# Kernel optimization log

Hardware: AMD Instinct MI355X
Metric: run time of the kernel (lower is better)

The kernel has to match this reference:

```python
import jax, jax.numpy as jnp
import numpy as np
from math import comb

ORDER = 16
K = ORDER + 1  # 17
D = 32         # input_dim
P = 20         # num_perm
N = 24576


def _bernstein(X, order):
    # X: [N, D] in [0,1] -> Bernstein basis [N, D, order+1]
    ks = jnp.arange(order + 1)
    binoms = jnp.array([comb(order, k) for k in range(order + 1)], jnp.float32)
    Xe = X[..., None]
    return (Xe ** ks) * ((1.0 - Xe) ** (order - ks)) * binoms


def _prior_sc_np(order):
    # prior_adjusting: sqrt(inv(B(x)^2) @ 1) at x = linspace(0,1,order+1)
    ks = np.arange(order + 1)
    binoms = np.array([comb(order, k) for k in range(order + 1)], np.float64)
    x = np.linspace(0.0, 1.0, order + 1)[:, None]
    B = (x ** ks) * ((1.0 - x) ** (order - ks)) * binoms  # (K, K)
    Pmat = np.linalg.inv(B ** 2)
    v = Pmat @ np.ones((order + 1, 1))
    return np.sqrt(np.maximum(v, 1e-12)).astype(np.float32)  # (K, 1)


def setup_inputs() -> dict:
    key = jax.random.key(0)
    k1, k2, k3, k4, k5 = jax.random.split(key, 5)
    mean_mu = (0.0001 / P) ** (1.0 / D)
    Xnew = jax.random.uniform(k1, (N, D), dtype=jnp.float32)
    meanw0 = mean_mu + 0.1 * jax.random.normal(k2, (P, 1, K), dtype=jnp.float32)
    meanw = mean_mu + 0.1 * jax.random.normal(k3, (D - 1, P, K, K), dtype=jnp.float32)
    varw0 = -0.1 + 0.1 * jax.random.normal(k4, (P, 1, K), dtype=jnp.float32)
    varw = -0.1 + 0.1 * jax.random.normal(k5, (D - 1, P, K, K), dtype=jnp.float32)
    rng = np.random.default_rng(0)
    perm = jnp.array(np.stack([rng.permutation(D) for _ in range(P)]), jnp.int32)
    prior_sc = jnp.array(_prior_sc_np(ORDER))
    post_prec = jnp.full((P,), float(P), dtype=jnp.float32)
    return {"Xnew": Xnew, "meanw0": meanw0, "meanw": meanw, "varw0": varw0,
            "varw": varw, "prior_sc": prior_sc, "post_prec": post_prec, "perm": perm}


def reference(Xnew, meanw0, meanw, varw0, varw, prior_sc, post_prec, perm):
    Bout = _bernstein(Xnew, ORDER)                      # (N, D, K)
    outB = jnp.transpose(Bout[:, perm], (1, 0, 2, 3))   # (P, N, D, K)
    outBd = jnp.transpose(outB, (2, 0, 1, 3))           # (D, P, N, K)

    # f_mean: ones(P,N,1) @ meanw0 -> broadcast of meanw0 rows; then chained small matmuls
    f0 = meanw0[:, 0, :][:, None, :] * outBd[0]         # (P, N, K)

    def mean_step(f, inputs):
        W, b = inputs                                   # W: (P,K,K), b: (P,N,K)
        return jnp.einsum('pnk,pkj->pnj', f, W) * b, None

    f, _ = jax.lax.scan(mean_step, f0, (meanw, outBd[1:]))
    f_mean = jnp.sum(jnp.sum(f, axis=-1), axis=0)[:, None]  # (N, 1)

    # f_var: weights exp(varw)*prior_sc^2.T, basis squared
    sc2 = (prior_sc ** 2)[:, 0]                          # (K,)
    g0 = (jnp.exp(varw0) * sc2)[:, 0, :][:, None, :] * outBd[0] ** 2  # (P, N, K)

    def var_step(g, inputs):
        Vw, b = inputs
        return jnp.einsum('pnk,pkj->pnj', g, jnp.exp(Vw) * sc2) * (b ** 2), None

    g, _ = jax.lax.scan(var_step, g0, (varw, outBd[1:]))
    f_var = jnp.sum(jnp.sum(g, axis=-1) / post_prec[:, None], axis=0)[:, None]  # (N, 1)
    return f_mean, f_var
```

## Files before the change

kernel.cpp:

```cpp
#include <hip/hip_runtime.h>

#define NN 24576
#define DD 32
#define KK 17
#define PP 20

__device__ __forceinline__ void bern17(float x, float* b) {
    const float binom[KK] = {1.f, 16.f, 120.f, 560.f, 1820.f, 4368.f, 8008.f, 11440.f,
                             12870.f, 11440.f, 8008.f, 4368.f, 1820.f, 560.f, 120.f, 16.f, 1.f};
    const float y = 1.0f - x;
    b[0] = 1.0f;
#pragma unroll
    for (int k = 1; k < KK; ++k) b[k] = b[k - 1] * x;
    float yp = 1.0f;
#pragma unroll
    for (int k = KK - 1; k >= 0; --k) {
        b[k] = b[k] * yp * binom[k];
        yp *= y;
    }
}

__global__ void prep_var(const float* __restrict__ varw, const float* __restrict__ varw0,
                         const float* __restrict__ prior_sc,
                         float* __restrict__ wv, float* __restrict__ wv0) {
    const int E1 = (DD - 1) * PP * KK * KK;
    int idx = blockIdx.x * blockDim.x + threadIdx.x;
    if (idx < E1) {
        int j = idx % KK;
        float s = prior_sc[j];
        wv[idx] = expf(varw[idx]) * s * s;
    } else if (idx < E1 + PP * KK) {
        int i = idx - E1;
        int k = i % KK;
        float s = prior_sc[k];
        wv0[i] = expf(varw0[i]) * s * s;
    }
}

__global__ void transpose_x(const float* __restrict__ X, float* __restrict__ XT) {
    __shared__ float t[32][33];
    const int n0 = blockIdx.x * 32;
    for (int r = threadIdx.y; r < 32; r += 8)
        t[r][threadIdx.x] = X[(n0 + r) * DD + threadIdx.x];
    __syncthreads();
    for (int d = threadIdx.y; d < 32; d += 8)
        XT[d * NN + n0 + threadIdx.x] = t[threadIdx.x][d];
}

__global__ __launch_bounds__(256, 4) void bez_chain2(
    const float* __restrict__ Xb,
    const int sx_d, const int sx_n,
    const float* __restrict__ mw0,
    const float* __restrict__ mW,
    const float* __restrict__ vw0,
    const float* __restrict__ vW,
    const float* __restrict__ post_prec,
    const int* __restrict__ perm,
    float* __restrict__ out)
{
    const bool VAR = (blockIdx.z != 0);
    const int p = blockIdx.y;
    const int n = blockIdx.x * blockDim.x + threadIdx.x;
    const int* __restrict__ pp = perm + p * DD;

    const float* __restrict__ w0 = (VAR ? vw0 : mw0);
    const float* __restrict__ W  = (VAR ? vW  : mW);

    float f[KK], b[KK];

    {
        const int pd = pp[0];
        const float x = Xb[pd * sx_d + n * sx_n];
        bern17(x, b);
        if (VAR) {
#pragma unroll
            for (int k = 0; k < KK; ++k) b[k] *= b[k];
        }
        const float* __restrict__ w0p = w0 + p * KK;
#pragma unroll
        for (int k = 0; k < KK; ++k) f[k] = w0p[k] * b[k];
    }

    for (int d = 1; d < DD; ++d) {
        const int pd = pp[d];
        const float x = Xb[pd * sx_d + n * sx_n];
        bern17(x, b);
        if (VAR) {
#pragma unroll
            for (int k = 0; k < KK; ++k) b[k] *= b[k];
        }

        const float* __restrict__ Wd = W + ((size_t)(d - 1) * PP + p) * (KK * KK);

        float fn[KK];
#pragma unroll
        for (int j = 0; j < KK; ++j) fn[j] = 0.0f;

#pragma unroll
        for (int k = 0; k < KK; ++k) {
            const float fk = f[k];
#pragma unroll
            for (int j = 0; j < KK; ++j)
                fn[j] = fmaf(fk, Wd[k * KK + j], fn[j]);
        }
#pragma unroll
        for (int j = 0; j < KK; ++j) f[j] = fn[j] * b[j];
    }

    float s = 0.0f;
#pragma unroll
    for (int j = 0; j < KK; ++j) s += f[j];
    if (VAR) s /= post_prec[p];

    atomicAdd(&out[(VAR ? NN : 0) + n], s);
}

extern "C" void kernel_launch(void* const* d_in, const int* in_sizes, int n_in,
                              void* d_out, int out_size, void* d_ws, size_t ws_size,
                              hipStream_t stream) {
    const float* X    = (const float*)d_in[0];
    const float* mw0  = (const float*)d_in[1];
    const float* mw   = (const float*)d_in[2];
    const float* vw0  = (const float*)d_in[3];
    const float* vw   = (const float*)d_in[4];
    const float* psc  = (const float*)d_in[5];
    const float* ppr  = (const float*)d_in[6];
    const int*   perm = (const int*)d_in[7];
    float* out = (float*)d_out;

    const size_t wv_elems  = (size_t)(DD - 1) * PP * KK * KK;
    const size_t wv0_elems = (size_t)PP * KK;
    const size_t xt_elems  = (size_t)DD * NN;

    float* wv  = (float*)d_ws;
    float* wv0 = wv + wv_elems;
    float* XT  = wv0 + wv0_elems;

    const size_t need = (wv_elems + wv0_elems + xt_elems) * sizeof(float);
    const bool use_xt = (ws_size >= need);

    hipMemsetAsync(d_out, 0, (size_t)out_size * sizeof(float), stream);

    const int E = (DD - 1) * PP * KK * KK + PP * KK;
    prep_var<<<dim3((E + 255) / 256), dim3(256), 0, stream>>>(vw, vw0, psc, wv, wv0);

    const float* Xb = X;
    int sx_d = 1, sx_n = DD;
    if (use_xt) {
        transpose_x<<<dim3(NN / 32), dim3(32, 8), 0, stream>>>(X, XT);
        Xb = XT; sx_d = NN; sx_n = 1;
    }

    dim3 grid(NN / 256, PP, 2), blk(256);
    bez_chain2<<<grid, blk, 0, stream>>>(Xb, sx_d, sx_n, mw0, mw, wv0, wv, ppr, perm, out);
}
```

Baseline: 301.1 us.

## Precompute Bernstein basis once per sample and share it across permutations

A new prep kernel evaluates the 17-term Bernstein basis for every (n, d) once and stores it in workspace in a coalesced [d][k][n] layout. The chain kernel then loads basis values instead of recomputing bern17 for each of the 40 mean/var chains. The grid is reordered so blocks for all permutations of the same sample range run close together, the d-loop is no longer unrolled, and launch bounds allow more occupancy. This trades per-chain ALU work for about 17x more memory traffic per basis read, and it chunks the work when the workspace is too small.

```diff
diff --git a/kernel.cpp b/kernel.cpp
--- a/kernel.cpp
+++ b/kernel.cpp
@@ -37,6 +37,95 @@
     }
 }
 
+__global__ void bern_prep(const float* __restrict__ X, float* __restrict__ B,
+                          const int n0, const int chunkN) {
+    const int i = blockIdx.x * blockDim.x + threadIdx.x;
+    if (i >= chunkN) return;
+    const int n = n0 + i;
+    float b[KK];
+    for (int d = 0; d < DD; ++d) {
+        const float x = X[(size_t)n * DD + d];
+        bern17(x, b);
+#pragma unroll
+        for (int k = 0; k < KK; ++k)
+            B[((size_t)d * KK + k) * chunkN + i] = b[k];
+    }
+}
+
+__global__ __launch_bounds__(256, 8) void bez_chainB(
+    const float* __restrict__ B, const int chunkN, const int n0,
+    const float* __restrict__ mw0,
+    const float* __restrict__ mW,
+    const float* __restrict__ vw0,
+    const float* __restrict__ vW,
+    const float* __restrict__ post_prec,
+    const int* __restrict__ perm,
+    float* __restrict__ out)
+{
+    const int bx = blockIdx.x;
+    const bool VAR = (bx >= PP);
+    const int p = VAR ? (bx - PP) : bx;
+    const int i = blockIdx.y * blockDim.x + threadIdx.x;
+    const int n = n0 + i;
+    const int* __restrict__ pp = perm + p * DD;
+
+    const float* __restrict__ w0 = VAR ? vw0 : mw0;
+    const float* __restrict__ W  = VAR ? vW  : mW;
+
+    float f[KK], bn[KK];
+
+    {
+        const int pd = pp[0];
+        const float* __restrict__ Bd = B + (size_t)pd * KK * chunkN + i;
+#pragma unroll
+        for (int k = 0; k < KK; ++k) bn[k] = Bd[(size_t)k * chunkN];
+        const float* __restrict__ w0p = w0 + p * KK;
+        if (VAR) {
+#pragma unroll
+            for (int k = 0; k < KK; ++k) f[k] = w0p[k] * (bn[k] * bn[k]);
+        } else {
+#pragma unroll
+            for (int k = 0; k < KK; ++k) f[k] = w0p[k] * bn[k];
+        }
+    }
+
+#pragma unroll 1
+    for (int d = 1; d < DD; ++d) {
+        const int pd = pp[d];
+        const float* __restrict__ Bd = B + (size_t)pd * KK * chunkN + i;
+#pragma unroll
+        for (int k = 0; k < KK; ++k) bn[k] = Bd[(size_t)k * chunkN];
+
+        const float* __restrict__ Wd = W + ((size_t)(d - 1) * PP + p) * (KK * KK);
+
+        float fn[KK];
+#pragma unroll
+        for (int j = 0; j < KK; ++j) fn[j] = f[0] * Wd[j];
+#pragma unroll
+        for (int k = 1; k < KK; ++k) {
+            const float fk = f[k];
+#pragma unroll
+            for (int j = 0; j < KK; ++j)
+                fn[j] = fmaf(fk, Wd[k * KK + j], fn[j]);
+        }
+
+        if (VAR) {
+#pragma unroll
+            for (int j = 0; j < KK; ++j) f[j] = fn[j] * (bn[j] * bn[j]);
+        } else {
+#pragma unroll
+            for (int j = 0; j < KK; ++j) f[j] = fn[j] * bn[j];
+        }
+    }
+
+    float s = 0.0f;
+#pragma unroll
+    for (int j = 0; j < KK; ++j) s += f[j];
+    if (VAR) s /= post_prec[p];
+
+    atomicAdd(&out[(VAR ? NN : 0) + n], s);
+}
+
 __global__ void transpose_x(const float* __restrict__ X, float* __restrict__ XT) {
     __shared__ float t[32][33];
     const int n0 = blockIdx.x * 32;
@@ -48,26 +137,20 @@
 }
 
 __global__ __launch_bounds__(256, 4) void bez_chain2(
-    const float* __restrict__ Xb,
-    const int sx_d, const int sx_n,
-    const float* __restrict__ mw0,
-    const float* __restrict__ mW,
-    const float* __restrict__ vw0,
-    const float* __restrict__ vW,
-    const float* __restrict__ post_prec,
-    const int* __restrict__ perm,
+    const float* __restrict__ Xb, const int sx_d, const int sx_n,
+    const float* __restrict__ mw0, const float* __restrict__ mW,
+    const float* __restrict__ vw0, const float* __restrict__ vW,
+    const float* __restrict__ post_prec, const int* __restrict__ perm,
     float* __restrict__ out)
 {
     const bool VAR = (blockIdx.z != 0);
     const int p = blockIdx.y;
     const int n = blockIdx.x * blockDim.x + threadIdx.x;
     const int* __restrict__ pp = perm + p * DD;
-
     const float* __restrict__ w0 = (VAR ? vw0 : mw0);
     const float* __restrict__ W  = (VAR ? vW  : mW);
 
     float f[KK], b[KK];
-
     {
         const int pd = pp[0];
         const float x = Xb[pd * sx_d + n * sx_n];
@@ -80,7 +163,6 @@
 #pragma unroll
         for (int k = 0; k < KK; ++k) f[k] = w0p[k] * b[k];
     }
-
     for (int d = 1; d < DD; ++d) {
         const int pd = pp[d];
         const float x = Xb[pd * sx_d + n * sx_n];
@@ -89,13 +171,10 @@
 #pragma unroll
             for (int k = 0; k < KK; ++k) b[k] *= b[k];
         }
-
         const float* __restrict__ Wd = W + ((size_t)(d - 1) * PP + p) * (KK * KK);
-
         float fn[KK];
 #pragma unroll
         for (int j = 0; j < KK; ++j) fn[j] = 0.0f;
-
 #pragma unroll
         for (int k = 0; k < KK; ++k) {
             const float fk = f[k];
@@ -106,12 +185,10 @@
 #pragma unroll
         for (int j = 0; j < KK; ++j) f[j] = fn[j] * b[j];
     }
-
     float s = 0.0f;
 #pragma unroll
     for (int j = 0; j < KK; ++j) s += f[j];
     if (VAR) s /= post_prec[p];
-
     atomicAdd(&out[(VAR ? NN : 0) + n], s);
 }
 
@@ -130,27 +207,42 @@
 
     const size_t wv_elems  = (size_t)(DD - 1) * PP * KK * KK;
     const size_t wv0_elems = (size_t)PP * KK;
-    const size_t xt_elems  = (size_t)DD * NN;
 
     float* wv  = (float*)d_ws;
     float* wv0 = wv + wv_elems;
-    float* XT  = wv0 + wv0_elems;
-
-    const size_t need = (wv_elems + wv0_elems + xt_elems) * sizeof(float);
-    const bool use_xt = (ws_size >= need);
+    float* Bws = wv0 + wv0_elems;
 
     hipMemsetAsync(d_out, 0, (size_t)out_size * sizeof(float), stream);
 
     const int E = (DD - 1) * PP * KK * KK + PP * KK;
     prep_var<<<dim3((E + 255) / 256), dim3(256), 0, stream>>>(vw, vw0, psc, wv, wv0);
 
-    const float* Xb = X;
-    int sx_d = 1, sx_n = DD;
-    if (use_xt) {
-        transpose_x<<<dim3(NN / 32), dim3(32, 8), 0, stream>>>(X, XT);
-        Xb = XT; sx_d = NN; sx_n = 1;
-    }
-
-    dim3 grid(NN / 256, PP, 2), blk(256);
-    bez_chain2<<<grid, blk, 0, stream>>>(Xb, sx_d, sx_n, mw0, mw, wv0, wv, ppr, perm, out);
-}
+    int nchunks = 0;
+    for (int c = 1; c <= 16; c *= 2) {
+        const size_t bElems = (size_t)DD * KK * (NN / c);
+        if ((wv_elems + wv0_elems + bElems) * sizeof(float) <= ws_size) { nchunks = c; break; }
+    }
+
+    if (nchunks > 0) {
+        const int chunkN = NN / nchunks;
+        for (int c = 0; c < nchunks; ++c) {
+            const int n0 = c * chunkN;
+            bern_prep<<<dim3((chunkN + 255) / 256), dim3(256), 0, stream>>>(X, Bws, n0, chunkN);
+            dim3 grid(2 * PP, chunkN / 256), blk(256);
+            bez_chainB<<<grid, blk, 0, stream>>>(Bws, chunkN, n0, mw0, mw, wv0, wv,
+                                                 ppr, perm, out);
+        }
+    } else {
+        const size_t xt_elems = (size_t)DD * NN;
+        const bool use_xt = ((wv_elems + wv0_elems + xt_elems) * sizeof(float) <= ws_size);
+        const float* Xb = X;
+        int sx_d = 1, sx_n = DD;
+        if (use_xt) {
+            float* XT = Bws;
+            transpose_x<<<dim3(NN / 32), dim3(32, 8), 0, stream>>>(X, XT);
+            Xb = XT; sx_d = NN; sx_n = 1;
+        }
+        dim3 grid(NN / 256, PP, 2), blk(256);
+        bez_chain2<<<grid, blk, 0, stream>>>(Xb, sx_d, sx_n, mw0, mw, wv0, wv, ppr, perm, out);
+    }
+}
```

Result: slower. 741.2 us (+146.2%).
